# Kernel tuning notes

Hardware: AMD Instinct MI355X
Metric: run time of the kernel (lower is better)

## Reference

```python
import jax, jax.numpy as jnp
import numpy as np


def setup_inputs() -> dict:
    key = jax.random.key(0)
    k1, k2, k3, k4 = jax.random.split(key, 4)
    H = 256
    std = 1.0 / np.sqrt(H)
    x = jax.random.normal(k1, (64, 512, 128), dtype=jnp.float32)
    Wi = jax.random.uniform(k2, (128, 4 * H), dtype=jnp.float32, minval=-std, maxval=std)
    Wh = jax.random.uniform(k3, (H, 4 * H), dtype=jnp.float32, minval=-std, maxval=std)
    B = jax.random.uniform(k4, (4 * H,), dtype=jnp.float32, minval=-std, maxval=std)
    return {"x": x, "Wi": Wi, "Wh": Wh, "B": B}


def reference(x, Wi, Wh, B):
    bs, seqs, _ = x.shape
    H = Wh.shape[0]
    h0 = jnp.zeros((bs, H), dtype=x.dtype)
    c0 = jnp.zeros((bs, H), dtype=x.dtype)
    # Precompute input projections for all timesteps: [bs, seqs, 4H]
    xproj = jnp.einsum('bsi,ig->bsg', x, Wi) + B

    def step(carry, xp_t):
        ht, ct = carry
        gates = xp_t + ht @ Wh  # [bs, 4H]
        it = jax.nn.sigmoid(gates[:, :H])
        ft = jax.nn.sigmoid(gates[:, H:2 * H])
        gt = jnp.tanh(gates[:, 2 * H:3 * H])
        ot = jax.nn.sigmoid(gates[:, 3 * H:])
        ct = ft * ct + it * gt
        ht = ot * jnp.tanh(ct)
        return (ht, ct), ht

    (ht, ct), hs = jax.lax.scan(step, (h0, c0), jnp.swapaxes(xproj, 0, 1))
    output = jnp.swapaxes(hs, 0, 1)  # [bs, seqs, H]
    return (output, (ht, ct))
```

## Files before the change

kernel.cpp:

```cpp
#include <hip/hip_runtime.h>
#include <hip/hip_bf16.h>

#define BATCH 64
#define SEQ   512
#define INPD  128
#define HID   256
#define G4    1024
#define PSS   272


#define HF(hv, rb) { \
    acc0 = fmaf(hv, wh[(rb)*8+0], acc0); acc1 = fmaf(hv, wh[(rb)*8+1], acc1); \
    acc2 = fmaf(hv, wh[(rb)*8+2], acc2); acc3 = fmaf(hv, wh[(rb)*8+3], acc3); \
    acc4 = fmaf(hv, wh[(rb)*8+4], acc4); acc5 = fmaf(hv, wh[(rb)*8+5], acc5); \
    acc6 = fmaf(hv, wh[(rb)*8+6], acc6); acc7 = fmaf(hv, wh[(rb)*8+7], acc7); }

#define XSET(xv) { \
    acc0 = xv * wi[0]; acc1 = xv * wi[1]; acc2 = xv * wi[2]; acc3 = xv * wi[3]; \
    acc4 = xv * wi[4]; acc5 = xv * wi[5]; acc6 = xv * wi[6]; acc7 = xv * wi[7]; }

#define XF(xv, rb) { \
    acc0 = fmaf(xv, wi[(rb)*8+0], acc0); acc1 = fmaf(xv, wi[(rb)*8+1], acc1); \
    acc2 = fmaf(xv, wi[(rb)*8+2], acc2); acc3 = fmaf(xv, wi[(rb)*8+3], acc3); \
    acc4 = fmaf(xv, wi[(rb)*8+4], acc4); acc5 = fmaf(xv, wi[(rb)*8+5], acc5); \
    acc6 = fmaf(xv, wi[(rb)*8+6], acc6); acc7 = fmaf(xv, wi[(rb)*8+7], acc7); }

#define XPART_ALL { \
    XSET(nx0.x) XF(nx0.y, 1) XF(nx0.z, 2) XF(nx0.w, 3) \
    XF(nx1.x, 4) XF(nx1.y, 5) XF(nx1.z, 6) XF(nx1.w, 7) }

__global__ __launch_bounds__(512, 2)
void ChaoticLSTM_kernel(const float* __restrict__ x,  const float* __restrict__ Wi,
                        const float* __restrict__ Wh, const float* __restrict__ Bb,
                        float* __restrict__ out, unsigned long long* __restrict__ exch)
{
    const int bid  = blockIdx.x;
    const int xcd  = bid & 7;
    const int slotn = bid >> 3;
    const int b    = xcd * 8 + (slotn >> 2);
    const int part = slotn & 3;
    const int tid  = threadIdx.x;
    const int CG   = tid >> 4;
    const int S    = tid & 15;
    const int g    = CG >> 3;
    const int jj0  = (CG & 7) * 8;
    const int gcol0 = g * 256 + part * 64 + jj0;

    __shared__ __align__(16) float h_lds[HID];
    __shared__ __align__(16) float ps[16 * PSS];
    __shared__ float act[256];

    float wh[128];
    float wi[64];
#pragma unroll
    for (int r = 0; r < 16; ++r) {
        const float* p = Wh + (size_t)(S * 16 + r) * G4 + gcol0;
        float4 u0 = *(const float4*)p;
        float4 u1 = *(const float4*)(p + 4);
        wh[r*8+0] = u0.x; wh[r*8+1] = u0.y; wh[r*8+2] = u0.z; wh[r*8+3] = u0.w;
        wh[r*8+4] = u1.x; wh[r*8+5] = u1.y; wh[r*8+6] = u1.z; wh[r*8+7] = u1.w;
    }
#pragma unroll
    for (int r = 0; r < 8; ++r) {
        const float* p = Wi + (size_t)(S * 8 + r) * G4 + gcol0;
        float4 u0 = *(const float4*)p;
        float4 u1 = *(const float4*)(p + 4);
        wi[r*8+0] = u0.x; wi[r*8+1] = u0.y; wi[r*8+2] = u0.z; wi[r*8+3] = u0.w;
        wi[r*8+4] = u1.x; wi[r*8+5] = u1.y; wi[r*8+6] = u1.z; wi[r*8+7] = u1.w;
    }
    const float Bred = (tid < 256) ? Bb[(tid >> 6) * 256 + part * 64 + (tid & 63)] : 0.f;

    unsigned long long* __restrict__ exb = exch + (size_t)b * 512;
    const float* __restrict__ xrow = x + (size_t)b * SEQ * INPD + S * 8;

    float cs = 0.f;
    if (tid < 256) h_lds[tid] = 0.f;
    if (tid < 64) {
        __hip_atomic_store(&exb[part*64 + tid],       0ull, __ATOMIC_RELAXED, __HIP_MEMORY_SCOPE_AGENT);
        __hip_atomic_store(&exb[256 + part*64 + tid], 0ull, __ATOMIC_RELAXED, __HIP_MEMORY_SCOPE_AGENT);
    }

    float acc0, acc1, acc2, acc3, acc4, acc5, acc6, acc7;
    {
        float4 nx0 = *(const float4*)(xrow);
        float4 nx1 = *(const float4*)(xrow + 4);
        XPART_ALL;
    }
    __syncthreads();

    for (int st = 0; st < SEQ; ++st) {
        const float* xp = xrow + (size_t)((st + 1 < SEQ) ? st + 1 : st) * INPD;
        float4 nx0 = *(const float4*)(xp);
        float4 nx1 = *(const float4*)(xp + 4);

        {
            float4 hv;
            hv = *(const float4*)(h_lds + S * 16);
            HF(hv.x, 0)  HF(hv.y, 1)  HF(hv.z, 2)  HF(hv.w, 3)
            hv = *(const float4*)(h_lds + S * 16 + 4);
            HF(hv.x, 4)  HF(hv.y, 5)  HF(hv.z, 6)  HF(hv.w, 7)
            hv = *(const float4*)(h_lds + S * 16 + 8);
            HF(hv.x, 8)  HF(hv.y, 9)  HF(hv.z, 10) HF(hv.w, 11)
            hv = *(const float4*)(h_lds + S * 16 + 12);
            HF(hv.x, 12) HF(hv.y, 13) HF(hv.z, 14) HF(hv.w, 15)
        }
        {
            float4 A = make_float4(acc0, acc1, acc2, acc3);
            float4 Bv = make_float4(acc4, acc5, acc6, acc7);
            *(float4*)(ps + S * PSS + CG * 8)     = A;
            *(float4*)(ps + S * PSS + CG * 8 + 4) = Bv;
        }
        __syncthreads();

        if (tid < 256) {
            const int c = tid;
            float t0 = ps[0*PSS+c]  + ps[1*PSS+c];
            float t1 = ps[2*PSS+c]  + ps[3*PSS+c];
            float t2 = ps[4*PSS+c]  + ps[5*PSS+c];
            float t3 = ps[6*PSS+c]  + ps[7*PSS+c];
            float t4 = ps[8*PSS+c]  + ps[9*PSS+c];
            float t5 = ps[10*PSS+c] + ps[11*PSS+c];
            float t6 = ps[12*PSS+c] + ps[13*PSS+c];
            float t7 = ps[14*PSS+c] + ps[15*PSS+c];
            float gs = Bred + (((t0 + t1) + (t2 + t3)) + ((t4 + t5) + (t6 + t7)));
            float a;
            if ((tid >> 6) == 2) a = tanhf(gs);
            else                 a = 1.f / (1.f + expf(-gs));
            act[c] = a;
        }
        __syncthreads();

        const unsigned tag = (unsigned)(st + 1);
        unsigned long long* slotp = exb + (st & 1) * 256;
        unsigned long long v = 0; int idx = 0;
        if (tid < 64) {
            float iv = act[tid], fv = act[64 + tid], gv = act[128 + tid], ov = act[192 + tid];
            cs = fv * cs + iv * gv;
            float hn = ov * tanhf(cs);
            int j = part * 64 + tid;
            unsigned long long w = ((unsigned long long)tag << 32)
                                 | (unsigned long long)__float_as_uint(hn);
            __hip_atomic_store(&slotp[j], w, __ATOMIC_RELAXED, __HIP_MEMORY_SCOPE_AGENT);
            h_lds[j] = hn;
            out[(size_t)(b * SEQ + st) * HID + j] = hn;
        } else if (tid < 256) {
            int q  = tid >> 6;
            int pp = (part + q) & 3;
            idx = pp * 64 + (tid & 63);
            v = __hip_atomic_load(&slotp[idx], __ATOMIC_RELAXED, __HIP_MEMORY_SCOPE_AGENT);
        }
        XPART_ALL;
        if (tid >= 64 && tid < 256) {
            while ((unsigned)(v >> 32) != tag)
                v = __hip_atomic_load(&slotp[idx], __ATOMIC_RELAXED, __HIP_MEMORY_SCOPE_AGENT);
            h_lds[idx] = __uint_as_float((unsigned)v);
        }
        __syncthreads();
    }

    if (tid < 64) {
        int j = part * 64 + tid;
        size_t base = (size_t)BATCH * SEQ * HID;
        out[base + (size_t)b * HID + j] = h_lds[j];
        out[base + (size_t)BATCH * HID + (size_t)b * HID + j] = cs;
    }
}

extern "C" void kernel_launch(void* const* d_in, const int* in_sizes, int n_in,
                              void* d_out, int out_size, void* d_ws, size_t ws_size,
                              hipStream_t stream) {
    const float* x  = (const float*)d_in[0];
    const float* Wi = (const float*)d_in[1];
    const float* Wh = (const float*)d_in[2];
    const float* B  = (const float*)d_in[3];
    float* out = (float*)d_out;
    unsigned long long* exch = (unsigned long long*)d_ws;

    ChaoticLSTM_kernel<<<dim3(256), dim3(512), 0, stream>>>(x, Wi, Wh, B, out, exch);
}
```

Before: 919.6 us.

## Reduce gate partials with wave shuffles and double-buffer hidden state

Each thread's partial sums are now combined across the 16 S-lanes with xor-shuffle butterflies, replacing the partial-sum LDS round trip. This removes one __syncthreads per step. The hidden state moves to a padded, double-buffered LDS array, so writes of the next h do not race with reads of the current one. Activations are computed by one lane per 16 for 8 columns each, which serialises more transcendental work per active thread. The last step also skips polling and the next-step input projection.

```diff
diff --git a/kernel.cpp b/kernel.cpp
--- a/kernel.cpp
+++ b/kernel.cpp
@@ -6,7 +6,8 @@
 #define INPD  128
 #define HID   256
 #define G4    1024
-#define PSS   272
+#define HPAD  68
+#define HBUFSZ (16 * HPAD)
 
 
 #define HF(hv, rb) { \
@@ -29,26 +30,31 @@
     XSET(nx0.x) XF(nx0.y, 1) XF(nx0.z, 2) XF(nx0.w, 3) \
     XF(nx1.x, 4) XF(nx1.y, 5) XF(nx1.z, 6) XF(nx1.w, 7) }
 
+#define BFLY(m) { \
+    acc0 += __shfl_xor(acc0, m); acc1 += __shfl_xor(acc1, m); \
+    acc2 += __shfl_xor(acc2, m); acc3 += __shfl_xor(acc3, m); \
+    acc4 += __shfl_xor(acc4, m); acc5 += __shfl_xor(acc5, m); \
+    acc6 += __shfl_xor(acc6, m); acc7 += __shfl_xor(acc7, m); }
+
 __global__ __launch_bounds__(512, 2)
 void ChaoticLSTM_kernel(const float* __restrict__ x,  const float* __restrict__ Wi,
                         const float* __restrict__ Wh, const float* __restrict__ Bb,
                         float* __restrict__ out, unsigned long long* __restrict__ exch)
 {
-    const int bid  = blockIdx.x;
-    const int xcd  = bid & 7;
+    const int bid   = blockIdx.x;
+    const int xcd   = bid & 7;
     const int slotn = bid >> 3;
-    const int b    = xcd * 8 + (slotn >> 2);
-    const int part = slotn & 3;
-    const int tid  = threadIdx.x;
-    const int CG   = tid >> 4;
-    const int S    = tid & 15;
-    const int g    = CG >> 3;
-    const int jj0  = (CG & 7) * 8;
+    const int b     = xcd * 8 + (slotn >> 2);
+    const int part  = slotn & 3;
+    const int tid   = threadIdx.x;
+    const int CG    = tid >> 4;
+    const int S     = tid & 15;
+    const int g     = CG >> 3;
+    const int jj0   = (CG & 7) * 8;
     const int gcol0 = g * 256 + part * 64 + jj0;
 
-    __shared__ __align__(16) float h_lds[HID];
-    __shared__ __align__(16) float ps[16 * PSS];
-    __shared__ float act[256];
+    __shared__ __align__(16) float hbuf[2][HBUFSZ];
+    __shared__ __align__(16) float act[256];
 
     float wh[128];
     float wi[64];
@@ -68,13 +74,14 @@
         wi[r*8+0] = u0.x; wi[r*8+1] = u0.y; wi[r*8+2] = u0.z; wi[r*8+3] = u0.w;
         wi[r*8+4] = u1.x; wi[r*8+5] = u1.y; wi[r*8+6] = u1.z; wi[r*8+7] = u1.w;
     }
-    const float Bred = (tid < 256) ? Bb[(tid >> 6) * 256 + part * 64 + (tid & 63)] : 0.f;
+    float4 bq0 = *(const float4*)(Bb + gcol0);
+    float4 bq1 = *(const float4*)(Bb + gcol0 + 4);
 
     unsigned long long* __restrict__ exb = exch + (size_t)b * 512;
     const float* __restrict__ xrow = x + (size_t)b * SEQ * INPD + S * 8;
 
-    float cs = 0.f;
-    if (tid < 256) h_lds[tid] = 0.f;
+    float cs = 0.f, hn_last = 0.f;
+    if (tid < 256) hbuf[0][(tid >> 4) * HPAD + (tid & 15)] = 0.f;
     if (tid < 64) {
         __hip_atomic_store(&exb[part*64 + tid],       0ull, __ATOMIC_RELAXED, __HIP_MEMORY_SCOPE_AGENT);
         __hip_atomic_store(&exb[256 + part*64 + tid], 0ull, __ATOMIC_RELAXED, __HIP_MEMORY_SCOPE_AGENT);
@@ -94,66 +101,64 @@
         float4 nx1 = *(const float4*)(xp + 4);
 
         {
+            const float* hb = hbuf[st & 1] + S * HPAD;
             float4 hv;
-            hv = *(const float4*)(h_lds + S * 16);
+            hv = *(const float4*)(hb);
             HF(hv.x, 0)  HF(hv.y, 1)  HF(hv.z, 2)  HF(hv.w, 3)
-            hv = *(const float4*)(h_lds + S * 16 + 4);
+            hv = *(const float4*)(hb + 4);
             HF(hv.x, 4)  HF(hv.y, 5)  HF(hv.z, 6)  HF(hv.w, 7)
-            hv = *(const float4*)(h_lds + S * 16 + 8);
+            hv = *(const float4*)(hb + 8);
             HF(hv.x, 8)  HF(hv.y, 9)  HF(hv.z, 10) HF(hv.w, 11)
-            hv = *(const float4*)(h_lds + S * 16 + 12);
+            hv = *(const float4*)(hb + 12);
             HF(hv.x, 12) HF(hv.y, 13) HF(hv.z, 14) HF(hv.w, 15)
         }
-        {
-            float4 A = make_float4(acc0, acc1, acc2, acc3);
-            float4 Bv = make_float4(acc4, acc5, acc6, acc7);
-            *(float4*)(ps + S * PSS + CG * 8)     = A;
-            *(float4*)(ps + S * PSS + CG * 8 + 4) = Bv;
-        }
-        __syncthreads();
+        BFLY(1) BFLY(2) BFLY(4) BFLY(8)
 
-        if (tid < 256) {
-            const int c = tid;
-            float t0 = ps[0*PSS+c]  + ps[1*PSS+c];
-            float t1 = ps[2*PSS+c]  + ps[3*PSS+c];
-            float t2 = ps[4*PSS+c]  + ps[5*PSS+c];
-            float t3 = ps[6*PSS+c]  + ps[7*PSS+c];
-            float t4 = ps[8*PSS+c]  + ps[9*PSS+c];
-            float t5 = ps[10*PSS+c] + ps[11*PSS+c];
-            float t6 = ps[12*PSS+c] + ps[13*PSS+c];
-            float t7 = ps[14*PSS+c] + ps[15*PSS+c];
-            float gs = Bred + (((t0 + t1) + (t2 + t3)) + ((t4 + t5) + (t6 + t7)));
-            float a;
-            if ((tid >> 6) == 2) a = tanhf(gs);
-            else                 a = 1.f / (1.f + expf(-gs));
-            act[c] = a;
+        if ((tid & 15) == 0) {
+            float s0 = acc0 + bq0.x, s1 = acc1 + bq0.y, s2 = acc2 + bq0.z, s3 = acc3 + bq0.w;
+            float s4 = acc4 + bq1.x, s5 = acc5 + bq1.y, s6 = acc6 + bq1.z, s7 = acc7 + bq1.w;
+            float a0, a1, a2, a3, a4, a5, a6, a7;
+            if (g == 2) {
+                a0 = tanhf(s0); a1 = tanhf(s1); a2 = tanhf(s2); a3 = tanhf(s3);
+                a4 = tanhf(s4); a5 = tanhf(s5); a6 = tanhf(s6); a7 = tanhf(s7);
+            } else {
+                a0 = 1.f/(1.f+expf(-s0)); a1 = 1.f/(1.f+expf(-s1));
+                a2 = 1.f/(1.f+expf(-s2)); a3 = 1.f/(1.f+expf(-s3));
+                a4 = 1.f/(1.f+expf(-s4)); a5 = 1.f/(1.f+expf(-s5));
+                a6 = 1.f/(1.f+expf(-s6)); a7 = 1.f/(1.f+expf(-s7));
+            }
+            *(float4*)(act + CG*8)     = make_float4(a0, a1, a2, a3);
+            *(float4*)(act + CG*8 + 4) = make_float4(a4, a5, a6, a7);
         }
         __syncthreads();
 
         const unsigned tag = (unsigned)(st + 1);
         unsigned long long* slotp = exb + (st & 1) * 256;
-        unsigned long long v = 0; int idx = 0;
+        float* hbn = hbuf[(st + 1) & 1];
         if (tid < 64) {
             float iv = act[tid], fv = act[64 + tid], gv = act[128 + tid], ov = act[192 + tid];
             cs = fv * cs + iv * gv;
             float hn = ov * tanhf(cs);
+            hn_last = hn;
             int j = part * 64 + tid;
             unsigned long long w = ((unsigned long long)tag << 32)
                                  | (unsigned long long)__float_as_uint(hn);
             __hip_atomic_store(&slotp[j], w, __ATOMIC_RELAXED, __HIP_MEMORY_SCOPE_AGENT);
-            h_lds[j] = hn;
+            hbn[(j >> 4) * HPAD + (tid & 15)] = hn;
             out[(size_t)(b * SEQ + st) * HID + j] = hn;
-        } else if (tid < 256) {
+        }
+        unsigned long long v = 0; int idx = 0;
+        const bool poller = (tid >= 64) && (tid < 256) && (st + 1 < SEQ);
+        if (poller) {
             int q  = tid >> 6;
-            int pp = (part + q) & 3;
-            idx = pp * 64 + (tid & 63);
+            idx = ((part + q) & 3) * 64 + (tid & 63);
             v = __hip_atomic_load(&slotp[idx], __ATOMIC_RELAXED, __HIP_MEMORY_SCOPE_AGENT);
         }
-        XPART_ALL;
-        if (tid >= 64 && tid < 256) {
+        if (st + 1 < SEQ) { XPART_ALL }
+        if (poller) {
             while ((unsigned)(v >> 32) != tag)
                 v = __hip_atomic_load(&slotp[idx], __ATOMIC_RELAXED, __HIP_MEMORY_SCOPE_AGENT);
-            h_lds[idx] = __uint_as_float((unsigned)v);
+            hbn[(idx >> 4) * HPAD + (idx & 15)] = __uint_as_float((unsigned)v);
         }
         __syncthreads();
     }
@@ -161,7 +166,7 @@
     if (tid < 64) {
         int j = part * 64 + tid;
         size_t base = (size_t)BATCH * SEQ * HID;
-        out[base + (size_t)b * HID + j] = h_lds[j];
+        out[base + (size_t)b * HID + j] = hn_last;
         out[base + (size_t)BATCH * HID + (size_t)b * HID + j] = cs;
     }
 }
```

Result: slower. 1.388 ms (+51.0%).

## Overlap input projection with gate activation phase and pad h LDS rows

Applied to the files above, without the earlier changes.

Threads 256-511, which sit idle while the gates are activated, now compute the next step's input projection in that phase instead of after it. The h vector in shared memory is stored in padded rows of 68 floats, and the partial-sum stride changes from 272 to 260, to reduce bank conflicts on the float4 reads. The spin-wait threads skip the exchange on the last step, and the final h is kept in a register. This moves work off the serial critical path between barriers, at the cost of more divergent code paths.

```diff
diff --git a/kernel.cpp b/kernel.cpp
--- a/kernel.cpp
+++ b/kernel.cpp
@@ -6,7 +6,8 @@
 #define INPD  128
 #define HID   256
 #define G4    1024
-#define PSS   272
+#define HPAD  68
+#define PSS   260
 
 
 #define HF(hv, rb) { \
@@ -34,21 +35,21 @@
                         const float* __restrict__ Wh, const float* __restrict__ Bb,
                         float* __restrict__ out, unsigned long long* __restrict__ exch)
 {
-    const int bid  = blockIdx.x;
-    const int xcd  = bid & 7;
+    const int bid   = blockIdx.x;
+    const int xcd   = bid & 7;
     const int slotn = bid >> 3;
-    const int b    = xcd * 8 + (slotn >> 2);
-    const int part = slotn & 3;
-    const int tid  = threadIdx.x;
-    const int CG   = tid >> 4;
-    const int S    = tid & 15;
-    const int g    = CG >> 3;
-    const int jj0  = (CG & 7) * 8;
+    const int b     = xcd * 8 + (slotn >> 2);
+    const int part  = slotn & 3;
+    const int tid   = threadIdx.x;
+    const int CG    = tid >> 4;
+    const int S     = tid & 15;
+    const int g     = CG >> 3;
+    const int jj0   = (CG & 7) * 8;
     const int gcol0 = g * 256 + part * 64 + jj0;
 
-    __shared__ __align__(16) float h_lds[HID];
+    __shared__ __align__(16) float hs[16 * HPAD];
     __shared__ __align__(16) float ps[16 * PSS];
-    __shared__ float act[256];
+    __shared__ __align__(16) float act[256];
 
     float wh[128];
     float wi[64];
@@ -73,8 +74,8 @@
     unsigned long long* __restrict__ exb = exch + (size_t)b * 512;
     const float* __restrict__ xrow = x + (size_t)b * SEQ * INPD + S * 8;
 
-    float cs = 0.f;
-    if (tid < 256) h_lds[tid] = 0.f;
+    float cs = 0.f, hn_last = 0.f;
+    if (tid < 256) hs[(tid >> 4) * HPAD + (tid & 15)] = 0.f;
     if (tid < 64) {
         __hip_atomic_store(&exb[part*64 + tid],       0ull, __ATOMIC_RELAXED, __HIP_MEMORY_SCOPE_AGENT);
         __hip_atomic_store(&exb[256 + part*64 + tid], 0ull, __ATOMIC_RELAXED, __HIP_MEMORY_SCOPE_AGENT);
@@ -94,22 +95,19 @@
         float4 nx1 = *(const float4*)(xp + 4);
 
         {
+            const float* hb = hs + S * HPAD;
             float4 hv;
-            hv = *(const float4*)(h_lds + S * 16);
+            hv = *(const float4*)(hb);
             HF(hv.x, 0)  HF(hv.y, 1)  HF(hv.z, 2)  HF(hv.w, 3)
-            hv = *(const float4*)(h_lds + S * 16 + 4);
+            hv = *(const float4*)(hb + 4);
             HF(hv.x, 4)  HF(hv.y, 5)  HF(hv.z, 6)  HF(hv.w, 7)
-            hv = *(const float4*)(h_lds + S * 16 + 8);
+            hv = *(const float4*)(hb + 8);
             HF(hv.x, 8)  HF(hv.y, 9)  HF(hv.z, 10) HF(hv.w, 11)
-            hv = *(const float4*)(h_lds + S * 16 + 12);
+            hv = *(const float4*)(hb + 12);
             HF(hv.x, 12) HF(hv.y, 13) HF(hv.z, 14) HF(hv.w, 15)
         }
-        {
-            float4 A = make_float4(acc0, acc1, acc2, acc3);
-            float4 Bv = make_float4(acc4, acc5, acc6, acc7);
-            *(float4*)(ps + S * PSS + CG * 8)     = A;
-            *(float4*)(ps + S * PSS + CG * 8 + 4) = Bv;
-        }
+        *(float4*)(ps + S * PSS + CG * 8)     = make_float4(acc0, acc1, acc2, acc3);
+        *(float4*)(ps + S * PSS + CG * 8 + 4) = make_float4(acc4, acc5, acc6, acc7);
         __syncthreads();
 
         if (tid < 256) {
@@ -127,33 +125,37 @@
             if ((tid >> 6) == 2) a = tanhf(gs);
             else                 a = 1.f / (1.f + expf(-gs));
             act[c] = a;
+        } else if (st + 1 < SEQ) {
+            XPART_ALL;
         }
         __syncthreads();
 
         const unsigned tag = (unsigned)(st + 1);
         unsigned long long* slotp = exb + (st & 1) * 256;
-        unsigned long long v = 0; int idx = 0;
         if (tid < 64) {
             float iv = act[tid], fv = act[64 + tid], gv = act[128 + tid], ov = act[192 + tid];
             cs = fv * cs + iv * gv;
             float hn = ov * tanhf(cs);
+            hn_last = hn;
             int j = part * 64 + tid;
             unsigned long long w = ((unsigned long long)tag << 32)
                                  | (unsigned long long)__float_as_uint(hn);
             __hip_atomic_store(&slotp[j], w, __ATOMIC_RELAXED, __HIP_MEMORY_SCOPE_AGENT);
-            h_lds[j] = hn;
+            hs[(j >> 4) * HPAD + (j & 15)] = hn;
             out[(size_t)(b * SEQ + st) * HID + j] = hn;
+            if (st + 1 < SEQ) { XPART_ALL }
         } else if (tid < 256) {
-            int q  = tid >> 6;
-            int pp = (part + q) & 3;
-            idx = pp * 64 + (tid & 63);
-            v = __hip_atomic_load(&slotp[idx], __ATOMIC_RELAXED, __HIP_MEMORY_SCOPE_AGENT);
-        }
-        XPART_ALL;
-        if (tid >= 64 && tid < 256) {
-            while ((unsigned)(v >> 32) != tag)
+            const bool live = (st + 1 < SEQ);
+            unsigned long long v = 0; int idx = 0;
+            if (live) {
+                int q  = tid >> 6;
+                idx = ((part + q) & 3) * 64 + (tid & 63);
                 v = __hip_atomic_load(&slotp[idx], __ATOMIC_RELAXED, __HIP_MEMORY_SCOPE_AGENT);
-            h_lds[idx] = __uint_as_float((unsigned)v);
+                XPART_ALL
+                while ((unsigned)(v >> 32) != tag)
+                    v = __hip_atomic_load(&slotp[idx], __ATOMIC_RELAXED, __HIP_MEMORY_SCOPE_AGENT);
+                hs[(idx >> 4) * HPAD + (idx & 15)] = __uint_as_float((unsigned)v);
+            }
         }
         __syncthreads();
     }
@@ -161,7 +163,7 @@
     if (tid < 64) {
         int j = part * 64 + tid;
         size_t base = (size_t)BATCH * SEQ * HID;
-        out[base + (size_t)b * HID + j] = h_lds[j];
+        out[base + (size_t)b * HID + j] = hn_last;
         out[base + (size_t)BATCH * HID + (size_t)b * HID + j] = cs;
     }
 }
```

After: 853.3 us. 7.2% less time.
